# Performance work log

Measured on AMD Instinct MI355X. Metric: run time of the kernel, lower is better.

Reference implementation:

```python
import jax, jax.numpy as jnp
import numpy as np

EPS = 1e-5

def rms_norm(x):
    # SimpleRMSNorm (no learned weight), as used inside BitLinear158
    return x * jax.lax.rsqrt(jnp.mean(x * x, axis=-1, keepdims=True) + EPS)

def act_quant(x):
    # int8 absmax quantization per last-dim row, with straight-through estimator
    scale = 127.0 / jnp.clip(jnp.max(jnp.abs(x), axis=-1, keepdims=True), 1e-5)
    q = jnp.clip(jnp.round(x * scale), -128.0, 127.0) / scale
    return x + jax.lax.stop_gradient(q - x)

def weight_quant(w):
    # ternary {-1,0,1} absmean quantization, with straight-through estimator
    scale = 1.0 / jnp.clip(jnp.mean(jnp.abs(w)), 1e-5)
    q = jnp.clip(jnp.round(w * scale), -1.0, 1.0) / scale
    return w + jax.lax.stop_gradient(q - w)

def bitlinear158(x, w, b):
    xq = act_quant(rms_norm(x))          # [b,s,d_in]
    wq = weight_quant(w)                 # [d_out,d_in]
    return jnp.einsum('bsd,od->bso', xq, wq) + b

def layer_norm(x, g, b):
    mu = jnp.mean(x, axis=-1, keepdims=True)
    var = jnp.mean((x - mu) ** 2, axis=-1, keepdims=True)
    return (x - mu) * jax.lax.rsqrt(var + EPS) * g + b

def setup_inputs() -> dict:
    key = jax.random.key(0)
    ks = jax.random.split(key, 3)
    d, inner = 2048, 8192
    x = jax.random.normal(ks[0], (4, 2048, d), dtype=jnp.float32)
    w1 = jax.random.normal(ks[1], (inner, d), dtype=jnp.float32) * 0.02
    b1 = jnp.zeros((inner,), jnp.float32)
    ln_g = jnp.ones((inner,), jnp.float32)
    ln_b = jnp.zeros((inner,), jnp.float32)
    w2 = jax.random.normal(ks[2], (d, inner), dtype=jnp.float32) * 0.02
    b2 = jnp.zeros((d,), jnp.float32)
    return {"x": x, "w1": w1, "b1": b1, "ln_g": ln_g, "ln_b": ln_b, "w2": w2, "b2": b2}

def reference(x, w1, b1, ln_g, ln_b, w2, b2):
    h = jax.nn.silu(bitlinear158(x, w1, b1))        # project_in: BitLinear158 + SiLU
    h = jax.nn.gelu(h, approximate=False)            # nn.GELU (exact erf form)
    h = layer_norm(h, ln_g, ln_b)                    # nn.LayerNorm(inner_dim)
    return bitlinear158(h, w2, b2)                   # BitLinear158 out projection
```

## Files before the change

### kernel.cpp

```cpp
#include <hip/hip_runtime.h>
#include <hip/hip_bf16.h>
#include <math.h>

typedef __bf16 bf16_t;
typedef __bf16 bf16x4 __attribute__((ext_vector_type(4)));
typedef int i32x4 __attribute__((ext_vector_type(4)));

#define AS1 __attribute__((address_space(1)))
#define AS3 __attribute__((address_space(3)))

__device__ __forceinline__ void gl_lds16(const char* g, char* l) {
  __builtin_amdgcn_global_load_lds((const AS1 void*)g, (AS3 void*)l, 16, 0, 0);
}

__device__ __forceinline__ unsigned pack4i(float a, float b, float c, float d) {
  return ((unsigned)(unsigned char)(int)a) | ((unsigned)(unsigned char)(int)b << 8) |
         ((unsigned)(unsigned char)(int)c << 16) | ((unsigned)(unsigned char)(int)d << 24);
}

__device__ __forceinline__ float block_sum_f(float v) {
  __shared__ float sb[4];
  #pragma unroll
  for (int o = 32; o; o >>= 1) v += __shfl_xor(v, o);
  if ((threadIdx.x & 63) == 0) sb[threadIdx.x >> 6] = v;
  __syncthreads();
  v = sb[0] + sb[1] + sb[2] + sb[3];
  __syncthreads();
  return v;
}
__device__ __forceinline__ float block_max_f(float v) {
  __shared__ float sm[4];
  #pragma unroll
  for (int o = 32; o; o >>= 1) v = fmaxf(v, __shfl_xor(v, o));
  if ((threadIdx.x & 63) == 0) sm[threadIdx.x >> 6] = v;
  __syncthreads();
  v = fmaxf(fmaxf(sm[0], sm[1]), fmaxf(sm[2], sm[3]));
  __syncthreads();
  return v;
}

__global__ __launch_bounds__(256) void wabs_partial(const float* __restrict__ w, int n4,
                                                    double* __restrict__ part) {
  const float4* w4 = (const float4*)w;
  double s = 0.0;
  const int stride = gridDim.x * blockDim.x;
  for (int i = blockIdx.x * blockDim.x + threadIdx.x; i < n4; i += stride) {
    float4 v = w4[i];
    s += (double)fabsf(v.x) + (double)fabsf(v.y) + (double)fabsf(v.z) + (double)fabsf(v.w);
  }
  #pragma unroll
  for (int o = 32; o; o >>= 1) s += __shfl_xor(s, o);
  __shared__ double sd[4];
  if ((threadIdx.x & 63) == 0) sd[threadIdx.x >> 6] = s;
  __syncthreads();
  if (threadIdx.x == 0) part[blockIdx.x] = sd[0] + sd[1] + sd[2] + sd[3];
}

__global__ __launch_bounds__(256) void wabs_final(const double* __restrict__ part, int np,
                                                  double n, float* __restrict__ fwout) {
  double s = 0.0;
  for (int i = threadIdx.x; i < np; i += blockDim.x) s += part[i];
  #pragma unroll
  for (int o = 32; o; o >>= 1) s += __shfl_xor(s, o);
  __shared__ double sd[4];
  if ((threadIdx.x & 63) == 0) sd[threadIdx.x >> 6] = s;
  __syncthreads();
  if (threadIdx.x == 0) {
    double mean = (sd[0] + sd[1] + sd[2] + sd[3]) / n;
    fwout[0] = (float)fmax(mean, 1e-5);
  }
}

__global__ __launch_bounds__(256) void quant_w(const float* __restrict__ w,
                                               const float* __restrict__ fw,
                                               char* __restrict__ wq, int n4) {
  int i = blockIdx.x * blockDim.x + threadIdx.x;
  if (i >= n4) return;
  const float s = 1.0f / fw[0];
  float4 v = ((const float4*)w)[i];
  ((unsigned*)wq)[i] = pack4i(fminf(fmaxf(rintf(v.x * s), -1.f), 1.f),
                              fminf(fmaxf(rintf(v.y * s), -1.f), 1.f),
                              fminf(fmaxf(rintf(v.z * s), -1.f), 1.f),
                              fminf(fmaxf(rintf(v.w * s), -1.f), 1.f));
}

__global__ __launch_bounds__(256) void rms_quant_x(const float* __restrict__ x,
                                                   char* __restrict__ xq,
                                                   float* __restrict__ fx, int K) {
  const int row = blockIdx.x, t = threadIdx.x;
  const size_t base = (size_t)row * K;
  float v[8];
  float ss = 0.f;
  #pragma unroll
  for (int j = 0; j < 2; j++) {
    float4 lv = *(const float4*)(x + base + j * 1024 + t * 4);
    v[j*4+0] = lv.x; v[j*4+1] = lv.y; v[j*4+2] = lv.z; v[j*4+3] = lv.w;
  }
  #pragma unroll
  for (int i = 0; i < 8; i++) ss += v[i] * v[i];
  ss = block_sum_f(ss);
  const float r = 1.0f / sqrtf(ss / (float)K + 1e-5f);
  float amax = 0.f;
  #pragma unroll
  for (int i = 0; i < 8; i++) { v[i] *= r; amax = fmaxf(amax, fabsf(v[i])); }
  amax = block_max_f(amax);
  amax = fmaxf(amax, 1e-5f);
  const float scale = 127.0f / amax;
  #pragma unroll
  for (int j = 0; j < 2; j++) {
    float q[4];
    #pragma unroll
    for (int e = 0; e < 4; e++)
      q[e] = fminf(fmaxf(rintf(v[j*4+e] * scale), -128.f), 127.f);
    *(unsigned*)(xq + base + j * 1024 + t * 4) = pack4i(q[0], q[1], q[2], q[3]);
  }
  if (t == 0) fx[row] = amax / 127.0f;
}

__global__ __launch_bounds__(256) void ln_rms_quant(const bf16_t* __restrict__ h,
                                                    char* __restrict__ hq,
                                                    const float* __restrict__ g,
                                                    const float* __restrict__ bb,
                                                    float* __restrict__ fh, int N) {
  const int row = blockIdx.x, t = threadIdx.x;
  const size_t base = (size_t)row * N;
  float v[32];
  float s = 0.f, ss = 0.f;
  #pragma unroll
  for (int j = 0; j < 8; j++) {
    const int col = j * 1024 + t * 4;
    bf16x4 q = *(const bf16x4*)(h + base + col);
    v[j*4+0] = (float)q[0]; v[j*4+1] = (float)q[1];
    v[j*4+2] = (float)q[2]; v[j*4+3] = (float)q[3];
  }
  #pragma unroll
  for (int i = 0; i < 32; i++) { s += v[i]; ss += v[i] * v[i]; }
  s = block_sum_f(s);
  ss = block_sum_f(ss);
  const float mu = s / (float)N;
  const float var = ss / (float)N - mu * mu;
  const float rstd = 1.0f / sqrtf(var + 1e-5f);
  float ss2 = 0.f;
  #pragma unroll
  for (int j = 0; j < 8; j++) {
    const int col = j * 1024 + t * 4;
    float4 gv = *(const float4*)(g + col);
    float4 bv = *(const float4*)(bb + col);
    float y0 = (v[j*4+0] - mu) * rstd * gv.x + bv.x;
    float y1 = (v[j*4+1] - mu) * rstd * gv.y + bv.y;
    float y2 = (v[j*4+2] - mu) * rstd * gv.z + bv.z;
    float y3 = (v[j*4+3] - mu) * rstd * gv.w + bv.w;
    v[j*4+0] = y0; v[j*4+1] = y1; v[j*4+2] = y2; v[j*4+3] = y3;
    ss2 += y0*y0 + y1*y1 + y2*y2 + y3*y3;
  }
  ss2 = block_sum_f(ss2);
  const float r2 = 1.0f / sqrtf(ss2 / (float)N + 1e-5f);
  float amax = 0.f;
  #pragma unroll
  for (int i = 0; i < 32; i++) { v[i] *= r2; amax = fmaxf(amax, fabsf(v[i])); }
  amax = block_max_f(amax);
  amax = fmaxf(amax, 1e-5f);
  const float scale = 127.0f / amax;
  #pragma unroll
  for (int j = 0; j < 8; j++) {
    const int col = j * 1024 + t * 4;
    float q[4];
    #pragma unroll
    for (int e = 0; e < 4; e++)
      q[e] = fminf(fmaxf(rintf(v[j*4+e] * scale), -128.f), 127.f);
    *(unsigned*)(hq + base + col) = pack4i(q[0], q[1], q[2], q[3]);
  }
  if (t == 0) fh[row] = amax / 127.0f;
}

template<int EPI, bool STORE_BF16>
__global__ __launch_bounds__(512, 2) void gemm256(const char* __restrict__ A,
                                                  const char* __restrict__ B,
                                                  const float* __restrict__ rowf,
                                                  const float* __restrict__ wf,
                                                  const float* __restrict__ bias,
                                                  float* __restrict__ Cf,
                                                  bf16_t* __restrict__ Cb,
                                                  int M, int N, int K) {
  __shared__ char smem[131072];

  const int ntile = N >> 8;
  const int cpx = gridDim.x >> 3;
  const int bid = blockIdx.x;
  const int xcd = bid & 7, local = bid >> 3;
  int wg;
  const int mrows = cpx / ntile;
  if (mrows * ntile == cpx && mrows > 0) {
    const int bm_l = local % mrows, bn_i = local / mrows;
    wg = (xcd * mrows + bm_l) * ntile + bn_i;
  } else {
    wg = xcd * cpx + local;
  }
  const int bm = wg / ntile, bn = wg % ntile;
  const int tm = bm << 8, tn = bn << 8;

  const int tid = threadIdx.x;
  const int w = tid >> 6, lane = tid & 63;
  const int wm = w >> 2, wn = w & 3;
  const int ln15 = lane & 15;

  const int srcRow = lane >> 2;
  const int srcCol = (((lane & 3) ^ ((lane >> 3) & 3)) << 4);
  const size_t KS = (size_t)K;
  const char* pAb = A + (size_t)(tm + w * 16 + srcRow) * KS + srcCol;
  const char* pBb = B + (size_t)(tn + w * 16 + srcRow) * KS + srcCol;
  const size_t hiO = (size_t)128 * KS;
  const int dA = w * 1024;

  const int foff = ln15 * 64 + ((((lane >> 4) ^ ((ln15 >> 1) & 3))) << 4);

  i32x4 acc[8][4] = {};
  const int NT = K >> 6;

#define SB __builtin_amdgcn_sched_barrier(0)
#define BAR { SB; __builtin_amdgcn_s_barrier(); SB; }
#define ST_ALL(bb, kt) { const size_t ko = (size_t)(kt) * 64;              \
    gl_lds16(pAb + ko,       smem + ((bb) << 15) + dA);                    \
    gl_lds16(pAb + hiO + ko, smem + ((bb) << 15) + 8192 + dA);             \
    gl_lds16(pBb + ko,       smem + ((bb) << 15) + 16384 + dA);            \
    gl_lds16(pBb + hiO + ko, smem + ((bb) << 15) + 16384 + 8192 + dA); }
#define MM(AF, BF, MB, NB)                                                   \
  _Pragma("unroll") for (int m4 = 0; m4 < 4; m4++)                           \
    _Pragma("unroll") for (int n2 = 0; n2 < 2; n2++)                         \
      acc[(MB)+m4][(NB)+n2] = __builtin_amdgcn_mfma_i32_16x16x64_i8(         \
          AF[m4], BF[n2], acc[(MB)+m4][(NB)+n2], 0, 0, 0);

  ST_ALL(0, 0); ST_ALL(1, 1); ST_ALL(2, 2);
  asm volatile("s_waitcnt vmcnt(8)" ::: "memory");
  BAR;

  int cur = 0;
  for (int t = 0; t < NT; ++t) {
    const int cb = cur << 15;
    const int stg = (cur + 3) & 3;
    if (t + 3 < NT) ST_ALL(stg, t + 3);
    SB;
    const char* sA = smem + cb;
    const char* sB = smem + cb + 16384;
    i32x4 afL[4], afH[4], bL[2], bH[2];
    #pragma unroll
    for (int m4 = 0; m4 < 4; m4++)
      afL[m4] = *(const i32x4*)(sA + (wm * 4 + m4) * 1024 + foff);
    #pragma unroll
    for (int n2 = 0; n2 < 2; n2++)
      bL[n2] = *(const i32x4*)(sB + (wn * 2 + n2) * 1024 + foff);
    #pragma unroll
    for (int m4 = 0; m4 < 4; m4++)
      afH[m4] = *(const i32x4*)(sA + 8192 + (wm * 4 + m4) * 1024 + foff);
    #pragma unroll
    for (int n2 = 0; n2 < 2; n2++)
      bH[n2] = *(const i32x4*)(sB + 8192 + (wn * 2 + n2) * 1024 + foff);
    __builtin_amdgcn_s_setprio(1);
    MM(afL, bL, 0, 0);
    MM(afH, bL, 4, 0);
    MM(afH, bH, 4, 2);
    MM(afL, bH, 0, 2);
    __builtin_amdgcn_s_setprio(0);
    if (t + 1 < NT) {
      if (t + 3 < NT)      asm volatile("s_waitcnt vmcnt(8)" ::: "memory");
      else if (t + 2 < NT) asm volatile("s_waitcnt vmcnt(4)" ::: "memory");
      else                 asm volatile("s_waitcnt vmcnt(0)" ::: "memory");
      BAR;
    }
    cur = (cur + 1) & 3;
  }
#undef ST_ALL
#undef MM

  const float fwv = wf[0];
  const int rq = (lane >> 4) << 2;
  float rsc[8][4];
  #pragma unroll
  for (int m = 0; m < 8; m++)
    #pragma unroll
    for (int r = 0; r < 4; r++)
      rsc[m][r] = rowf[tm + (m >> 2) * 128 + wm * 64 + (m & 3) * 16 + rq + r] * fwv;

  #pragma unroll
  for (int m = 0; m < 8; m++) {
    #pragma unroll
    for (int n = 0; n < 4; n++) {
      const int col = tn + (n >> 1) * 128 + wn * 32 + (n & 1) * 16 + ln15;
      const float bv = bias[col];
      #pragma unroll
      for (int r = 0; r < 4; r++) {
        const int row = tm + (m >> 2) * 128 + wm * 64 + (m & 3) * 16 + rq + r;
        float val = (float)acc[m][n][r] * rsc[m][r] + bv;
        if (EPI == 1) {
          float sl = val / (1.0f + expf(-val));
          val = 0.5f * sl * (1.0f + erff(sl * 0.70710678118654752f));
        }
        if (STORE_BF16) Cb[(size_t)row * N + col] = (bf16_t)val;
        else            Cf[(size_t)row * N + col] = val;
      }
    }
  }
}

extern "C" void kernel_launch(void* const* d_in, const int* in_sizes, int n_in,
                              void* d_out, int out_size, void* d_ws, size_t ws_size,
                              hipStream_t stream) {
  const float* x   = (const float*)d_in[0];
  const float* w1  = (const float*)d_in[1];
  const float* b1  = (const float*)d_in[2];
  const float* lng = (const float*)d_in[3];
  const float* lnb = (const float*)d_in[4];
  const float* w2  = (const float*)d_in[5];
  const float* b2  = (const float*)d_in[6];
  float* out = (float*)d_out;

  const int inner = in_sizes[2];
  const int d     = in_sizes[1] / inner;
  const int M     = in_sizes[0] / d;

  char* ws = (char*)d_ws;
  size_t off = 0;
  double* part = (double*)(ws + off); off += 1024 * 8;
  float*  fw   = (float*)(ws + off);  off += 256;
  float*  fx   = (float*)(ws + off);  off += (size_t)M * 4;
  float*  fh   = (float*)(ws + off);  off += (size_t)M * 4;
  char*   w1q  = ws + off;            off += (size_t)inner * d;
  char*   w2q  = ws + off;            off += (size_t)inner * d;

  int MC = M;
  while (MC > 256 && off + (size_t)MC * ((size_t)d + 3 * (size_t)inner) > ws_size) MC >>= 1;
  char*   xq = ws + off;              off += (size_t)MC * d;
  bf16_t* h  = (bf16_t*)(ws + off);   off += (size_t)MC * inner * 2;
  char*   hq = ws + off;

  const int nw = inner * d;
  const int n4 = nw / 4;

  wabs_partial<<<1024, 256, 0, stream>>>(w1, n4, part);
  wabs_final<<<1, 256, 0, stream>>>(part, 1024, (double)nw, fw + 0);
  wabs_partial<<<1024, 256, 0, stream>>>(w2, n4, part);
  wabs_final<<<1, 256, 0, stream>>>(part, 1024, (double)nw, fw + 1);
  quant_w<<<n4 / 256, 256, 0, stream>>>(w1, fw + 0, w1q, n4);
  quant_w<<<n4 / 256, 256, 0, stream>>>(w2, fw + 1, w2q, n4);

  for (int mc = 0; mc < M; mc += MC) {
    rms_quant_x<<<MC, 256, 0, stream>>>(x + (size_t)mc * d, xq, fx, d);

    const int g1 = (MC / 256) * (inner / 256);
    gemm256<1, true><<<g1, 512, 0, stream>>>(xq, w1q, fx, fw + 0, b1,
                                             nullptr, h, MC, inner, d);

    ln_rms_quant<<<MC, 256, 0, stream>>>(h, hq, lng, lnb, fh, inner);

    const int g2 = (MC / 256) * (d / 256);
    gemm256<0, false><<<g2, 512, 0, stream>>>(hq, w2q, fh, fw + 1, b2,
                                              out + (size_t)mc * d, nullptr, MC, d, inner);
  }
}
```

Before: 468.0 us.

## Restructure int8 GEMM mainloop to BK=128 double-buffered, quarter-staged loads

Raises the K-tile from 64 to 128 bytes and replaces the 4-stage ring buffer with two buffers. Each buffer is split into A-lo, A-hi, B-lo and B-hi quarters that are loaded and consumed in an interleaved schedule with a barrier between sub-phases. The LDS swizzle changes to an 8-way XOR for the 128-byte rows. The intent is to halve loop iterations and overlap the global-to-LDS copies with the MFMA work at a finer grain. The epilogue also swaps expf for __expf. The trade-off is more barriers per iteration and a shallower prefetch depth, which can expose memory latency.

```diff
diff --git a/kernel.cpp b/kernel.cpp
--- a/kernel.cpp
+++ b/kernel.cpp
@@ -204,73 +204,92 @@
   const int wm = w >> 2, wn = w & 3;
   const int ln15 = lane & 15;
 
-  const int srcRow = lane >> 2;
-  const int srcCol = (((lane & 3) ^ ((lane >> 3) & 3)) << 4);
+  const int srow = lane >> 3;
+  const int scol = ((lane & 7) ^ srow) << 4;
   const size_t KS = (size_t)K;
-  const char* pAb = A + (size_t)(tm + w * 16 + srcRow) * KS + srcCol;
-  const char* pBb = B + (size_t)(tn + w * 16 + srcRow) * KS + srcCol;
+  const char* pAst = A + (size_t)(tm + w * 16 + srow) * KS + scol;
+  const char* pBst = B + (size_t)(tn + w * 16 + srow) * KS + scol;
   const size_t hiO = (size_t)128 * KS;
-  const int dA = w * 1024;
-
-  const int foff = ln15 * 64 + ((((lane >> 4) ^ ((ln15 >> 1) & 3))) << 4);
+  const size_t r8 = (size_t)8 * KS;
+  const int dW = w * 2048;
+
+  int foffk[2];
+  #pragma unroll
+  for (int kk = 0; kk < 2; kk++)
+    foffk[kk] = ln15 * 128 + ((((kk << 2) + (lane >> 4)) ^ (ln15 & 7)) << 4);
 
   i32x4 acc[8][4] = {};
-  const int NT = K >> 6;
+  const int NT = K >> 7;
 
 #define SB __builtin_amdgcn_sched_barrier(0)
 #define BAR { SB; __builtin_amdgcn_s_barrier(); SB; }
-#define ST_ALL(bb, kt) { const size_t ko = (size_t)(kt) * 64;              \
-    gl_lds16(pAb + ko,       smem + ((bb) << 15) + dA);                    \
-    gl_lds16(pAb + hiO + ko, smem + ((bb) << 15) + 8192 + dA);             \
-    gl_lds16(pBb + ko,       smem + ((bb) << 15) + 16384 + dA);            \
-    gl_lds16(pBb + hiO + ko, smem + ((bb) << 15) + 16384 + 8192 + dA); }
+#define ST_A(bb, hh, kt) { const char* p = pAst + ((hh) ? hiO : 0) + (size_t)(kt) * 128; \
+    char* dst = smem + (bb) * 32768 + (hh) * 16384 + dW;                                 \
+    gl_lds16(p, dst); gl_lds16(p + r8, dst + 1024); }
+#define ST_B(bb, hh, kt) { const char* p = pBst + ((hh) ? hiO : 0) + (size_t)(kt) * 128; \
+    char* dst = smem + 65536 + (bb) * 32768 + (hh) * 16384 + dW;                         \
+    gl_lds16(p, dst); gl_lds16(p + r8, dst + 1024); }
 #define MM(AF, BF, MB, NB)                                                   \
-  _Pragma("unroll") for (int m4 = 0; m4 < 4; m4++)                           \
-    _Pragma("unroll") for (int n2 = 0; n2 < 2; n2++)                         \
-      acc[(MB)+m4][(NB)+n2] = __builtin_amdgcn_mfma_i32_16x16x64_i8(         \
-          AF[m4], BF[n2], acc[(MB)+m4][(NB)+n2], 0, 0, 0);
-
-  ST_ALL(0, 0); ST_ALL(1, 1); ST_ALL(2, 2);
-  asm volatile("s_waitcnt vmcnt(8)" ::: "memory");
-  BAR;
-
-  int cur = 0;
+  _Pragma("unroll") for (int kk = 0; kk < 2; kk++)                           \
+    _Pragma("unroll") for (int m4 = 0; m4 < 4; m4++)                         \
+      _Pragma("unroll") for (int n2 = 0; n2 < 2; n2++)                       \
+        acc[(MB)+m4][(NB)+n2] = __builtin_amdgcn_mfma_i32_16x16x64_i8(       \
+            AF[m4][kk], BF[n2][kk], acc[(MB)+m4][(NB)+n2], 0, 0, 0);
+#define VM(n) asm volatile("s_waitcnt vmcnt(" #n ")" ::: "memory")
+
+  ST_A(0, 0, 0); ST_B(0, 0, 0); ST_B(0, 1, 0); ST_A(0, 1, 0);
+
   for (int t = 0; t < NT; ++t) {
-    const int cb = cur << 15;
-    const int stg = (cur + 3) & 3;
-    if (t + 3 < NT) ST_ALL(stg, t + 3);
-    SB;
-    const char* sA = smem + cb;
-    const char* sB = smem + cb + 16384;
-    i32x4 afL[4], afH[4], bL[2], bH[2];
+    const int b = t & 1, nb = b ^ 1;
+    const char* sA = smem + b * 32768;
+    const char* sB = smem + 65536 + b * 32768;
+    i32x4 afL[4][2], afH[4][2], bL[2][2], bH[2][2];
+    if (t + 1 < NT) { ST_A(nb, 0, t + 1); ST_B(nb, 0, t + 1); VM(8); }
+    else            { VM(4); }
+    BAR;
     #pragma unroll
     for (int m4 = 0; m4 < 4; m4++)
-      afL[m4] = *(const i32x4*)(sA + (wm * 4 + m4) * 1024 + foff);
+      #pragma unroll
+      for (int kk = 0; kk < 2; kk++)
+        afL[m4][kk] = *(const i32x4*)(sA + (wm * 4 + m4) * 2048 + foffk[kk]);
     #pragma unroll
     for (int n2 = 0; n2 < 2; n2++)
-      bL[n2] = *(const i32x4*)(sB + (wn * 2 + n2) * 1024 + foff);
-    #pragma unroll
-    for (int m4 = 0; m4 < 4; m4++)
-      afH[m4] = *(const i32x4*)(sA + 8192 + (wm * 4 + m4) * 1024 + foff);
-    #pragma unroll
-    for (int n2 = 0; n2 < 2; n2++)
-      bH[n2] = *(const i32x4*)(sB + 8192 + (wn * 2 + n2) * 1024 + foff);
+      #pragma unroll
+      for (int kk = 0; kk < 2; kk++)
+        bL[n2][kk] = *(const i32x4*)(sB + (wn * 2 + n2) * 2048 + foffk[kk]);
     __builtin_amdgcn_s_setprio(1);
     MM(afL, bL, 0, 0);
-    MM(afH, bL, 4, 0);
-    MM(afH, bH, 4, 2);
+    __builtin_amdgcn_s_setprio(0);
+    if (t + 1 < NT) { ST_B(nb, 1, t + 1); VM(8); }
+    else            { VM(2); }
+    BAR;
+    #pragma unroll
+    for (int n2 = 0; n2 < 2; n2++)
+      #pragma unroll
+      for (int kk = 0; kk < 2; kk++)
+        bH[n2][kk] = *(const i32x4*)(sB + 16384 + (wn * 2 + n2) * 2048 + foffk[kk]);
+    __builtin_amdgcn_s_setprio(1);
     MM(afL, bH, 0, 2);
     __builtin_amdgcn_s_setprio(0);
-    if (t + 1 < NT) {
-      if (t + 3 < NT)      asm volatile("s_waitcnt vmcnt(8)" ::: "memory");
-      else if (t + 2 < NT) asm volatile("s_waitcnt vmcnt(4)" ::: "memory");
-      else                 asm volatile("s_waitcnt vmcnt(0)" ::: "memory");
-      BAR;
-    }
-    cur = (cur + 1) & 3;
-  }
-#undef ST_ALL
+    if (t + 1 < NT) { ST_A(nb, 1, t + 1); VM(8); }
+    else            { VM(0); }
+    BAR;
+    #pragma unroll
+    for (int m4 = 0; m4 < 4; m4++)
+      #pragma unroll
+      for (int kk = 0; kk < 2; kk++)
+        afH[m4][kk] = *(const i32x4*)(sA + 16384 + (wm * 4 + m4) * 2048 + foffk[kk]);
+    __builtin_amdgcn_s_setprio(1);
+    MM(afH, bH, 4, 2);
+    __builtin_amdgcn_s_setprio(0);
+    __builtin_amdgcn_s_setprio(1);
+    MM(afH, bL, 4, 0);
+    __builtin_amdgcn_s_setprio(0);
+  }
+#undef ST_A
+#undef ST_B
 #undef MM
+#undef VM
 
   const float fwv = wf[0];
   const int rq = (lane >> 4) << 2;
@@ -292,7 +311,7 @@
         const int row = tm + (m >> 2) * 128 + wm * 64 + (m & 3) * 16 + rq + r;
         float val = (float)acc[m][n][r] * rsc[m][r] + bv;
         if (EPI == 1) {
-          float sl = val / (1.0f + expf(-val));
+          float sl = val / (1.0f + __expf(-val));
           val = 0.5f * sl * (1.0f + erff(sl * 0.70710678118654752f));
         }
         if (STORE_BF16) Cb[(size_t)row * N + col] = (bf16_t)val;
```

Result: faster. 433.7 us (-7.3%).

## Shrink int8 GEMM tile to 256x128 with 4 waves and triple-buffered LDS

Applied to the files above, without the earlier changes.

Changes the int8 MFMA GEMM from 256x256 tiles with 8 waves and a 4-stage LDS pipeline to 256x128 tiles with 4 waves, each wave computing a 128x64 sub-tile, using a 3-stage buffer in 72KB of LDS. The barrier and wait now come at the top of each iteration, with the prefetch issued two stages ahead. It aims to raise occupancy and block count (more blocks per GEMM, less LDS per block) at the cost of lower per-block data reuse and more B-side reloads. The SiLU epilogue also switches to the fast __expf intrinsic.

```diff
diff --git a/kernel.cpp b/kernel.cpp
--- a/kernel.cpp
+++ b/kernel.cpp
@@ -174,7 +174,7 @@
 }
 
 template<int EPI, bool STORE_BF16>
-__global__ __launch_bounds__(512, 2) void gemm256(const char* __restrict__ A,
+__global__ __launch_bounds__(256, 2) void gemm256(const char* __restrict__ A,
                                                   const char* __restrict__ B,
                                                   const float* __restrict__ rowf,
                                                   const float* __restrict__ wf,
@@ -182,9 +182,9 @@
                                                   float* __restrict__ Cf,
                                                   bf16_t* __restrict__ Cb,
                                                   int M, int N, int K) {
-  __shared__ char smem[131072];
-
-  const int ntile = N >> 8;
+  __shared__ char smem[73728];
+
+  const int ntile = N >> 7;
   const int cpx = gridDim.x >> 3;
   const int bid = blockIdx.x;
   const int xcd = bid & 7, local = bid >> 3;
@@ -197,20 +197,20 @@
     wg = xcd * cpx + local;
   }
   const int bm = wg / ntile, bn = wg % ntile;
-  const int tm = bm << 8, tn = bn << 8;
+  const int tm = bm << 8, tn = bn << 7;
 
   const int tid = threadIdx.x;
   const int w = tid >> 6, lane = tid & 63;
-  const int wm = w >> 2, wn = w & 3;
+  const int wm = w >> 1, wn = w & 1;
   const int ln15 = lane & 15;
 
-  const int srcRow = lane >> 2;
-  const int srcCol = (((lane & 3) ^ ((lane >> 3) & 3)) << 4);
+  const int srow = lane >> 2;
+  const int scol = (((lane & 3) ^ ((lane >> 3) & 3)) << 4);
   const size_t KS = (size_t)K;
-  const char* pAb = A + (size_t)(tm + w * 16 + srcRow) * KS + srcCol;
-  const char* pBb = B + (size_t)(tn + w * 16 + srcRow) * KS + srcCol;
-  const size_t hiO = (size_t)128 * KS;
-  const int dA = w * 1024;
+  const char* pAst = A + (size_t)(tm + w * 16 + srow) * KS + scol;
+  const char* pBst = B + (size_t)(tn + w * 16 + srow) * KS + scol;
+  const size_t r64 = (size_t)64 * KS;
+  const int dW = w * 1024;
 
   const int foff = ln15 * 64 + ((((lane >> 4) ^ ((ln15 >> 1) & 3))) << 4);
 
@@ -219,58 +219,46 @@
 
 #define SB __builtin_amdgcn_sched_barrier(0)
 #define BAR { SB; __builtin_amdgcn_s_barrier(); SB; }
-#define ST_ALL(bb, kt) { const size_t ko = (size_t)(kt) * 64;              \
-    gl_lds16(pAb + ko,       smem + ((bb) << 15) + dA);                    \
-    gl_lds16(pAb + hiO + ko, smem + ((bb) << 15) + 8192 + dA);             \
-    gl_lds16(pBb + ko,       smem + ((bb) << 15) + 16384 + dA);            \
-    gl_lds16(pBb + hiO + ko, smem + ((bb) << 15) + 16384 + 8192 + dA); }
-#define MM(AF, BF, MB, NB)                                                   \
-  _Pragma("unroll") for (int m4 = 0; m4 < 4; m4++)                           \
-    _Pragma("unroll") for (int n2 = 0; n2 < 2; n2++)                         \
-      acc[(MB)+m4][(NB)+n2] = __builtin_amdgcn_mfma_i32_16x16x64_i8(         \
-          AF[m4], BF[n2], acc[(MB)+m4][(NB)+n2], 0, 0, 0);
-
-  ST_ALL(0, 0); ST_ALL(1, 1); ST_ALL(2, 2);
-  asm volatile("s_waitcnt vmcnt(8)" ::: "memory");
-  BAR;
+#define VM(n) asm volatile("s_waitcnt vmcnt(" #n ")" ::: "memory")
+#define ST(bb, kt) { const size_t ko = (size_t)(kt) * 64;                    \
+    char* ab = smem + (bb) * 24576 + dW;                                     \
+    char* bbp = smem + (bb) * 24576 + 16384 + dW;                            \
+    gl_lds16(pAst + ko,            ab);                                      \
+    gl_lds16(pAst + r64 + ko,      ab + 4096);                               \
+    gl_lds16(pAst + 2 * r64 + ko,  ab + 8192);                               \
+    gl_lds16(pAst + 3 * r64 + ko,  ab + 12288);                              \
+    gl_lds16(pBst + ko,            bbp);                                     \
+    gl_lds16(pBst + r64 + ko,      bbp + 4096); }
+
+  ST(0, 0); ST(1, 1);
 
   int cur = 0;
   for (int t = 0; t < NT; ++t) {
-    const int cb = cur << 15;
-    const int stg = (cur + 3) & 3;
-    if (t + 3 < NT) ST_ALL(stg, t + 3);
-    SB;
-    const char* sA = smem + cb;
-    const char* sB = smem + cb + 16384;
-    i32x4 afL[4], afH[4], bL[2], bH[2];
-    #pragma unroll
-    for (int m4 = 0; m4 < 4; m4++)
-      afL[m4] = *(const i32x4*)(sA + (wm * 4 + m4) * 1024 + foff);
-    #pragma unroll
-    for (int n2 = 0; n2 < 2; n2++)
-      bL[n2] = *(const i32x4*)(sB + (wn * 2 + n2) * 1024 + foff);
-    #pragma unroll
-    for (int m4 = 0; m4 < 4; m4++)
-      afH[m4] = *(const i32x4*)(sA + 8192 + (wm * 4 + m4) * 1024 + foff);
-    #pragma unroll
-    for (int n2 = 0; n2 < 2; n2++)
-      bH[n2] = *(const i32x4*)(sB + 8192 + (wn * 2 + n2) * 1024 + foff);
+    if (t + 1 < NT) { VM(6); } else { VM(0); }
+    BAR;
+    int s2 = cur + 2; if (s2 >= 3) s2 -= 3;
+    if (t + 2 < NT) ST(s2, t + 2);
+    const char* sA = smem + cur * 24576;
+    const char* sBp = sA + 16384;
+    i32x4 afr[8], bfr[4];
+    #pragma unroll
+    for (int m4 = 0; m4 < 8; m4++)
+      afr[m4] = *(const i32x4*)(sA + (wm * 8 + m4) * 1024 + foff);
+    #pragma unroll
+    for (int n2 = 0; n2 < 4; n2++)
+      bfr[n2] = *(const i32x4*)(sBp + (wn * 4 + n2) * 1024 + foff);
     __builtin_amdgcn_s_setprio(1);
-    MM(afL, bL, 0, 0);
-    MM(afH, bL, 4, 0);
-    MM(afH, bH, 4, 2);
-    MM(afL, bH, 0, 2);
+    #pragma unroll
+    for (int m4 = 0; m4 < 8; m4++)
+      #pragma unroll
+      for (int n2 = 0; n2 < 4; n2++)
+        acc[m4][n2] = __builtin_amdgcn_mfma_i32_16x16x64_i8(afr[m4], bfr[n2],
+                                                            acc[m4][n2], 0, 0, 0);
     __builtin_amdgcn_s_setprio(0);
-    if (t + 1 < NT) {
-      if (t + 3 < NT)      asm volatile("s_waitcnt vmcnt(8)" ::: "memory");
-      else if (t + 2 < NT) asm volatile("s_waitcnt vmcnt(4)" ::: "memory");
-      else                 asm volatile("s_waitcnt vmcnt(0)" ::: "memory");
-      BAR;
-    }
-    cur = (cur + 1) & 3;
-  }
-#undef ST_ALL
-#undef MM
+    cur = cur + 1 == 3 ? 0 : cur + 1;
+  }
+#undef ST
+#undef VM
 
   const float fwv = wf[0];
   const int rq = (lane >> 4) << 2;
@@ -279,20 +267,20 @@
   for (int m = 0; m < 8; m++)
     #pragma unroll
     for (int r = 0; r < 4; r++)
-      rsc[m][r] = rowf[tm + (m >> 2) * 128 + wm * 64 + (m & 3) * 16 + rq + r] * fwv;
+      rsc[m][r] = rowf[tm + wm * 128 + m * 16 + rq + r] * fwv;
 
   #pragma unroll
   for (int m = 0; m < 8; m++) {
     #pragma unroll
     for (int n = 0; n < 4; n++) {
-      const int col = tn + (n >> 1) * 128 + wn * 32 + (n & 1) * 16 + ln15;
+      const int col = tn + wn * 64 + n * 16 + ln15;
       const float bv = bias[col];
       #pragma unroll
       for (int r = 0; r < 4; r++) {
-        const int row = tm + (m >> 2) * 128 + wm * 64 + (m & 3) * 16 + rq + r;
+        const int row = tm + wm * 128 + m * 16 + rq + r;
         float val = (float)acc[m][n][r] * rsc[m][r] + bv;
         if (EPI == 1) {
-          float sl = val / (1.0f + expf(-val));
+          float sl = val / (1.0f + __expf(-val));
           val = 0.5f * sl * (1.0f + erff(sl * 0.70710678118654752f));
         }
         if (STORE_BF16) Cb[(size_t)row * N + col] = (bf16_t)val;
@@ -346,14 +334,14 @@
   for (int mc = 0; mc < M; mc += MC) {
     rms_quant_x<<<MC, 256, 0, stream>>>(x + (size_t)mc * d, xq, fx, d);
 
-    const int g1 = (MC / 256) * (inner / 256);
-    gemm256<1, true><<<g1, 512, 0, stream>>>(xq, w1q, fx, fw + 0, b1,
+    const int g1 = (MC / 256) * (inner / 128);
+    gemm256<1, true><<<g1, 256, 0, stream>>>(xq, w1q, fx, fw + 0, b1,
                                              nullptr, h, MC, inner, d);
 
     ln_rms_quant<<<MC, 256, 0, stream>>>(h, hq, lng, lnb, fh, inner);
 
-    const int g2 = (MC / 256) * (d / 256);
-    gemm256<0, false><<<g2, 512, 0, stream>>>(hq, w2q, fh, fw + 1, b2,
+    const int g2 = (MC / 256) * (d / 128);
+    gemm256<0, false><<<g2, 256, 0, stream>>>(hq, w2q, fh, fw + 1, b2,
                                               out + (size_t)mc * d, nullptr, MC, d, inner);
   }
 }
```

After: 460.2 us. About the same (-1.7%).

## Restructure int8 GEMM main loop into 3-stage, two-phase interleaved pipeline

Applied to the files above, without the earlier changes.

Cuts the LDS ring from four to three 32KB stages and splits each K-step into two half-phases. Each phase issues part of the next global->LDS prefetch, reads its fragments and runs half of the MFMAs, with extra barriers and lgkmcnt waits in between. The goal is to overlap fragment loads and prefetch with MFMA work, and the smaller LDS footprint could fit more blocks per CU. The cost is a shallower prefetch depth and more barriers per iteration. SiLU in the epilogue also switches to the fast __expf intrinsic.

```diff
diff --git a/kernel.cpp b/kernel.cpp
--- a/kernel.cpp
+++ b/kernel.cpp
@@ -182,7 +182,7 @@
                                                   float* __restrict__ Cf,
                                                   bf16_t* __restrict__ Cb,
                                                   int M, int N, int K) {
-  __shared__ char smem[131072];
+  __shared__ char smem[98304];
 
   const int ntile = N >> 8;
   const int cpx = gridDim.x >> 3;
@@ -204,13 +204,13 @@
   const int wm = w >> 2, wn = w & 3;
   const int ln15 = lane & 15;
 
-  const int srcRow = lane >> 2;
-  const int srcCol = (((lane & 3) ^ ((lane >> 3) & 3)) << 4);
+  const int srow = lane >> 2;
+  const int scol = (((lane & 3) ^ ((lane >> 3) & 3)) << 4);
   const size_t KS = (size_t)K;
-  const char* pAb = A + (size_t)(tm + w * 16 + srcRow) * KS + srcCol;
-  const char* pBb = B + (size_t)(tn + w * 16 + srcRow) * KS + srcCol;
-  const size_t hiO = (size_t)128 * KS;
-  const int dA = w * 1024;
+  const char* pAst = A + (size_t)(tm + w * 16 + srow) * KS + scol;
+  const char* pBst = B + (size_t)(tn + w * 16 + srow) * KS + scol;
+  const size_t r128 = (size_t)128 * KS;
+  const int dW = w * 1024;
 
   const int foff = ln15 * 64 + ((((lane >> 4) ^ ((ln15 >> 1) & 3))) << 4);
 
@@ -219,58 +219,68 @@
 
 #define SB __builtin_amdgcn_sched_barrier(0)
 #define BAR { SB; __builtin_amdgcn_s_barrier(); SB; }
-#define ST_ALL(bb, kt) { const size_t ko = (size_t)(kt) * 64;              \
-    gl_lds16(pAb + ko,       smem + ((bb) << 15) + dA);                    \
-    gl_lds16(pAb + hiO + ko, smem + ((bb) << 15) + 8192 + dA);             \
-    gl_lds16(pBb + ko,       smem + ((bb) << 15) + 16384 + dA);            \
-    gl_lds16(pBb + hiO + ko, smem + ((bb) << 15) + 16384 + 8192 + dA); }
+#define LGKM0 { asm volatile("s_waitcnt lgkmcnt(0)" ::: "memory"); SB; }
+#define VM(n) asm volatile("s_waitcnt vmcnt(" #n ")" ::: "memory")
+#define ST_A(bb, kt) { const size_t ko = (size_t)(kt) * 64;                  \
+    gl_lds16(pAst + ko,        smem + (bb) * 32768 + dW);                    \
+    gl_lds16(pAst + r128 + ko, smem + (bb) * 32768 + 8192 + dW); }
+#define ST_B(bb, kt) { const size_t ko = (size_t)(kt) * 64;                  \
+    gl_lds16(pBst + ko,        smem + (bb) * 32768 + 16384 + dW);            \
+    gl_lds16(pBst + r128 + ko, smem + (bb) * 32768 + 16384 + 8192 + dW); }
 #define MM(AF, BF, MB, NB)                                                   \
   _Pragma("unroll") for (int m4 = 0; m4 < 4; m4++)                           \
     _Pragma("unroll") for (int n2 = 0; n2 < 2; n2++)                         \
       acc[(MB)+m4][(NB)+n2] = __builtin_amdgcn_mfma_i32_16x16x64_i8(         \
           AF[m4], BF[n2], acc[(MB)+m4][(NB)+n2], 0, 0, 0);
 
-  ST_ALL(0, 0); ST_ALL(1, 1); ST_ALL(2, 2);
-  asm volatile("s_waitcnt vmcnt(8)" ::: "memory");
+  ST_A(0, 0); ST_B(0, 0);
+  ST_A(1, 1); ST_B(1, 1);
+  VM(4);
   BAR;
 
   int cur = 0;
   for (int t = 0; t < NT; ++t) {
-    const int cb = cur << 15;
-    const int stg = (cur + 3) & 3;
-    if (t + 3 < NT) ST_ALL(stg, t + 3);
-    SB;
-    const char* sA = smem + cb;
-    const char* sB = smem + cb + 16384;
+    int s2 = cur + 2; if (s2 >= 3) s2 -= 3;
+    const char* sA = smem + cur * 32768;
+    const char* sB = sA + 16384;
     i32x4 afL[4], afH[4], bL[2], bH[2];
+    #pragma unroll
+    for (int n2 = 0; n2 < 2; n2++)
+      bL[n2] = *(const i32x4*)(sB + (wn * 2 + n2) * 1024 + foff);
     #pragma unroll
     for (int m4 = 0; m4 < 4; m4++)
       afL[m4] = *(const i32x4*)(sA + (wm * 4 + m4) * 1024 + foff);
     #pragma unroll
     for (int n2 = 0; n2 < 2; n2++)
-      bL[n2] = *(const i32x4*)(sB + (wn * 2 + n2) * 1024 + foff);
+      bH[n2] = *(const i32x4*)(sB + 8192 + (wn * 2 + n2) * 1024 + foff);
+    if (t + 2 < NT) ST_A(s2, t + 2);
+    SB;
+    BAR;
+    LGKM0;
+    __builtin_amdgcn_s_setprio(1);
+    MM(afL, bL, 0, 0);
+    MM(afL, bH, 0, 2);
+    __builtin_amdgcn_s_setprio(0);
+    BAR;
     #pragma unroll
     for (int m4 = 0; m4 < 4; m4++)
       afH[m4] = *(const i32x4*)(sA + 8192 + (wm * 4 + m4) * 1024 + foff);
-    #pragma unroll
-    for (int n2 = 0; n2 < 2; n2++)
-      bH[n2] = *(const i32x4*)(sB + 8192 + (wn * 2 + n2) * 1024 + foff);
+    if (t + 2 < NT) { ST_B(s2, t + 2); VM(4); }
+    else if (t + 1 < NT) { VM(0); }
+    SB;
+    BAR;
+    LGKM0;
     __builtin_amdgcn_s_setprio(1);
-    MM(afL, bL, 0, 0);
+    MM(afH, bH, 4, 2);
     MM(afH, bL, 4, 0);
-    MM(afH, bH, 4, 2);
-    MM(afL, bH, 0, 2);
     __builtin_amdgcn_s_setprio(0);
-    if (t + 1 < NT) {
-      if (t + 3 < NT)      asm volatile("s_waitcnt vmcnt(8)" ::: "memory");
-      else if (t + 2 < NT) asm volatile("s_waitcnt vmcnt(4)" ::: "memory");
-      else                 asm volatile("s_waitcnt vmcnt(0)" ::: "memory");
-      BAR;
-    }
-    cur = (cur + 1) & 3;
-  }
-#undef ST_ALL
+    BAR;
+    cur = cur + 1 == 3 ? 0 : cur + 1;
+  }
+#undef ST_A
+#undef ST_B
 #undef MM
+#undef VM
 
   const float fwv = wf[0];
   const int rq = (lane >> 4) << 2;
@@ -292,7 +302,7 @@
         const int row = tm + (m >> 2) * 128 + wm * 64 + (m & 3) * 16 + rq + r;
         float val = (float)acc[m][n][r] * rsc[m][r] + bv;
         if (EPI == 1) {
-          float sl = val / (1.0f + expf(-val));
+          float sl = val / (1.0f + __expf(-val));
           val = 0.5f * sl * (1.0f + erff(sl * 0.70710678118654752f));
         }
         if (STORE_BF16) Cb[(size_t)row * N + col] = (bf16_t)val;
```

New measurement: 453.6 us. -3.1%, faster.
